# Performance work log

Measured on AMD Instinct MI355X. Metric: run time of the kernel, lower is better.

The kernel has to match this reference:

```python
import jax, jax.numpy as jnp
import numpy as np

DEPTH = 4
DIM = 1024
HEADS = 16
DIM_HEAD = 64
INNER = HEADS * DIM_HEAD  # 1024
MLP = 4096
CTX = 768
SCALE = DIM_HEAD ** -0.5
EPS = 1e-5


def setup_inputs() -> dict:
    key = jax.random.key(0)
    ks = jax.random.split(key, 12)
    def rn(k, shape, s=0.02):
        return jax.random.normal(k, shape, jnp.float32) * s
    return {
        "x": jax.random.normal(ks[0], (2, 2048, DIM), jnp.float32),
        "context": jax.random.normal(ks[1], (2, 1024, CTX), jnp.float32),
        "ln1_g": jnp.ones((DEPTH, DIM), jnp.float32),
        "ln1_b": jnp.zeros((DEPTH, DIM), jnp.float32),
        "w_qkv": rn(ks[2], (DEPTH, DIM, 3 * INNER)),
        "w_sa_o": rn(ks[3], (DEPTH, INNER, DIM)),
        "b_sa_o": jnp.zeros((DEPTH, DIM), jnp.float32),
        "ln2_g": jnp.ones((DEPTH, DIM), jnp.float32),
        "ln2_b": jnp.zeros((DEPTH, DIM), jnp.float32),
        "w_q": rn(ks[4], (DEPTH, DIM, INNER)),
        "w_kv": rn(ks[5], (DEPTH, CTX, 2 * INNER)),
        "w_ca_o": rn(ks[6], (DEPTH, INNER, DIM)),
        "b_ca_o": jnp.zeros((DEPTH, DIM), jnp.float32),
        "ln3_g": jnp.ones((DEPTH, DIM), jnp.float32),
        "ln3_b": jnp.zeros((DEPTH, DIM), jnp.float32),
        "w_ff1": rn(ks[7], (DEPTH, DIM, MLP)),
        "b_ff1": jnp.zeros((DEPTH, MLP), jnp.float32),
        "w_ff2": rn(ks[8], (DEPTH, MLP, DIM)),
        "b_ff2": jnp.zeros((DEPTH, DIM), jnp.float32),
    }


def _ln(x, g, b):
    mu = jnp.mean(x, axis=-1, keepdims=True)
    var = jnp.mean(jnp.square(x - mu), axis=-1, keepdims=True)
    return (x - mu) * jax.lax.rsqrt(var + EPS) * g + b


def _heads(t):
    # [b, n, h*d] -> [b, h, n, d]
    b, n, _ = t.shape
    return t.reshape(b, n, HEADS, DIM_HEAD).transpose(0, 2, 1, 3)


def _mha(q, k, v):
    # q,k,v: [b, h, n, d]; naive matmul-softmax-matmul, same math as the torch code
    attn = jax.nn.softmax(jnp.einsum('bhqd,bhkd->bhqk', q, k) * SCALE, axis=-1)
    out = jnp.einsum('bhqk,bhkd->bhqd', attn, v)
    b, h, n, d = out.shape
    return out.transpose(0, 2, 1, 3).reshape(b, n, h * d)


def reference(x, context, ln1_g, ln1_b, w_qkv, w_sa_o, b_sa_o,
              ln2_g, ln2_b, w_q, w_kv, w_ca_o, b_ca_o,
              ln3_g, ln3_b, w_ff1, b_ff1, w_ff2, b_ff2):
    for i in range(DEPTH):
        # self-attention
        h = _ln(x, ln1_g[i], ln1_b[i])
        qkv = h @ w_qkv[i]
        q, k, v = jnp.split(qkv, 3, axis=-1)
        sa = _mha(_heads(q), _heads(k), _heads(v)) @ w_sa_o[i] + b_sa_o[i]
        x = sa + x
        # cross-attention
        h = _ln(x, ln2_g[i], ln2_b[i])
        q = h @ w_q[i]
        kv = context @ w_kv[i]
        k, v = jnp.split(kv, 2, axis=-1)
        ca = _mha(_heads(q), _heads(k), _heads(v)) @ w_ca_o[i] + b_ca_o[i]
        x = ca + x
        # feed-forward (exact GELU, matching torch nn.GELU default)
        h = _ln(x, ln3_g[i], ln3_b[i])
        ff = jax.nn.gelu(h @ w_ff1[i] + b_ff1[i], approximate=False) @ w_ff2[i] + b_ff2[i]
        x = ff + x
    return x
```

## Files before the change

### kernel.cpp

```cpp
#include <hip/hip_runtime.h>
#include <hip/hip_bf16.h>
#include <math.h>

typedef __bf16 bf16_t;
typedef __bf16 bf16x8 __attribute__((ext_vector_type(8)));
typedef __bf16 bf16x4 __attribute__((ext_vector_type(4)));
typedef float f32x4 __attribute__((ext_vector_type(4)));
typedef unsigned short u16;
typedef unsigned int u32;
typedef u16 u16x8 __attribute__((ext_vector_type(8)));

#define NDEPTH 4
#define DIM 1024
#define NHEADS 16
#define MLP_DIM 4096
#define CTXD 768
#define NTOK 4096
#define NCTX 2048
#define ATT_SCALE 0.125f

__device__ inline void gload_lds16(const void* g, void* l) {
  __builtin_amdgcn_global_load_lds(
      (const __attribute__((address_space(1))) void*)g,
      (__attribute__((address_space(3))) void*)l, 16, 0, 0);
}

__device__ inline u32 packbf2(float a, float b) {
  union { bf16_t h[2]; u32 w; } u;
  u.h[0] = (bf16_t)a; u.h[1] = (bf16_t)b;
  return u.w;
}

template<int EPI>
__device__ inline void epi_store(void* outp, const float* bias, const float* res,
                                 int row, int col, int N, float v) {
  size_t idx = (size_t)row * N + col;
  if (EPI == 3) {
    ((float*)outp)[idx] = v + bias[col] + res[idx];
  } else if (EPI == 2) {
    float vb = v + bias[col];
    ((bf16_t*)outp)[idx] = (bf16_t)(0.5f * vb * (1.f + erff(vb * 0.70710678118f)));
  } else {
    ((bf16_t*)outp)[idx] = (bf16_t)v;
  }
}

template<int EPI>
__global__ __launch_bounds__(512) void gemm_bf16(
    const bf16_t* __restrict__ A, const bf16_t* __restrict__ Bt,
    const float* __restrict__ bias, const float* __restrict__ res,
    void* __restrict__ outp, int M, int N, int K)
{
  __shared__ alignas(16) bf16_t As[3][128 * 32];
  __shared__ alignas(16) bf16_t Bs[3][128 * 32];
  const int tid = threadIdx.x, lane = tid & 63, wave = tid >> 6;
  const int bx = blockIdx.x, by = blockIdx.y;
  const int wr = wave >> 2, wc = wave & 3;
  const int l15 = lane & 15, l4 = lane >> 4;

  const bf16_t* Ag = A + (size_t)by * 128 * K;
  const bf16_t* Bg = Bt + (size_t)bx * 128 * K;

  f32x4 acc[4][2] = {};

  const int srow = tid >> 2, soff = (tid & 3) * 8;
  auto stage = [&](int buf, int k0) {
    gload_lds16(Ag + (size_t)srow * K + k0 + soff, &As[buf][(size_t)tid * 8]);
    gload_lds16(Bg + (size_t)srow * K + k0 + soff, &Bs[buf][(size_t)tid * 8]);
  };

  const int nk = K >> 5;
  stage(0, 0);
  stage(1, 32);
  asm volatile("s_waitcnt vmcnt(2)" ::: "memory");
  __builtin_amdgcn_s_barrier();
  __builtin_amdgcn_sched_barrier(0);

  for (int t = 0; t < nk; ++t) {
    const int cur = t % 3;
    if (t + 2 < nk) stage((t + 2) % 3, (t + 2) << 5);

    bf16x8 af[4], bfr[2];
#pragma unroll
    for (int mi = 0; mi < 4; ++mi)
      af[mi] = *(const bf16x8*)&As[cur][(wr * 64 + mi * 16 + l15) * 32 + l4 * 8];
#pragma unroll
    for (int ni = 0; ni < 2; ++ni)
      bfr[ni] = *(const bf16x8*)&Bs[cur][(wc * 32 + ni * 16 + l15) * 32 + l4 * 8];
#pragma unroll
    for (int mi = 0; mi < 4; ++mi)
#pragma unroll
      for (int ni = 0; ni < 2; ++ni)
        acc[mi][ni] = __builtin_amdgcn_mfma_f32_16x16x32_bf16(af[mi], bfr[ni], acc[mi][ni], 0, 0, 0);

    if (t + 2 < nk) {
      asm volatile("s_waitcnt vmcnt(2)" ::: "memory");
    } else if (t + 1 < nk) {
      asm volatile("s_waitcnt vmcnt(0)" ::: "memory");
    } else {
      break;
    }
    __builtin_amdgcn_s_barrier();
    __builtin_amdgcn_sched_barrier(0);
  }

  const int r0 = by * 128 + wr * 64, c0 = bx * 128 + wc * 32;
#pragma unroll
  for (int ni = 0; ni < 2; ++ni)
#pragma unroll
    for (int mi = 0; mi < 4; ++mi)
#pragma unroll
      for (int r = 0; r < 4; ++r)
        epi_store<EPI>(outp, bias, res, r0 + mi * 16 + l4 * 4 + r,
                       c0 + ni * 16 + l15, N, acc[mi][ni][r]);
}

template<int EPI>
__global__ __launch_bounds__(256) void gemm64_bf16(
    const bf16_t* __restrict__ A, const bf16_t* __restrict__ Bt,
    const float* __restrict__ bias, const float* __restrict__ res,
    void* __restrict__ outp, int M, int N, int K)
{
  __shared__ alignas(16) bf16_t As[3][64 * 32];
  __shared__ alignas(16) bf16_t Bs[3][64 * 32];
  const int tid = threadIdx.x, lane = tid & 63, wave = tid >> 6;
  const int bx = blockIdx.x, by = blockIdx.y;
  const int wr = wave >> 1, wc = wave & 1;
  const int l15 = lane & 15, l4 = lane >> 4;

  const bf16_t* Ag = A + (size_t)by * 64 * K;
  const bf16_t* Bg = Bt + (size_t)bx * 64 * K;

  f32x4 acc[2][2] = {};

  const int srow = tid >> 2, soff = (tid & 3) * 8;
  auto stage = [&](int buf, int k0) {
    gload_lds16(Ag + (size_t)srow * K + k0 + soff, &As[buf][(size_t)tid * 8]);
    gload_lds16(Bg + (size_t)srow * K + k0 + soff, &Bs[buf][(size_t)tid * 8]);
  };

  const int nk = K >> 5;
  stage(0, 0);
  stage(1, 32);
  asm volatile("s_waitcnt vmcnt(2)" ::: "memory");
  __builtin_amdgcn_s_barrier();
  __builtin_amdgcn_sched_barrier(0);

  for (int t = 0; t < nk; ++t) {
    const int cur = t % 3;
    if (t + 2 < nk) stage((t + 2) % 3, (t + 2) << 5);

    bf16x8 af[2], bfr[2];
#pragma unroll
    for (int mi = 0; mi < 2; ++mi)
      af[mi] = *(const bf16x8*)&As[cur][(wr * 32 + mi * 16 + l15) * 32 + l4 * 8];
#pragma unroll
    for (int ni = 0; ni < 2; ++ni)
      bfr[ni] = *(const bf16x8*)&Bs[cur][(wc * 32 + ni * 16 + l15) * 32 + l4 * 8];
#pragma unroll
    for (int mi = 0; mi < 2; ++mi)
#pragma unroll
      for (int ni = 0; ni < 2; ++ni)
        acc[mi][ni] = __builtin_amdgcn_mfma_f32_16x16x32_bf16(af[mi], bfr[ni], acc[mi][ni], 0, 0, 0);

    if (t + 2 < nk) {
      asm volatile("s_waitcnt vmcnt(2)" ::: "memory");
    } else if (t + 1 < nk) {
      asm volatile("s_waitcnt vmcnt(0)" ::: "memory");
    } else {
      break;
    }
    __builtin_amdgcn_s_barrier();
    __builtin_amdgcn_sched_barrier(0);
  }

  const int r0 = by * 64 + wr * 32, c0 = bx * 64 + wc * 32;
#pragma unroll
  for (int ni = 0; ni < 2; ++ni)
#pragma unroll
    for (int mi = 0; mi < 2; ++mi)
#pragma unroll
      for (int r = 0; r < 4; ++r)
        epi_store<EPI>(outp, bias, res, r0 + mi * 16 + l4 * 4 + r,
                       c0 + ni * 16 + l15, N, acc[mi][ni][r]);
}

__global__ __launch_bounds__(512) void attn_fwd(
    const bf16_t* __restrict__ Q, int qs,
    const bf16_t* __restrict__ K, const bf16_t* __restrict__ V, int kvs,
    bf16_t* __restrict__ O, int os, int nq, int nk)
{
  __shared__ bf16_t Ks[2][64][72];
  __shared__ bf16_t Vt[2][64][72];

  const int tid = threadIdx.x, lane = tid & 63, wv = tid >> 6;
  const int l15 = lane & 15, l4 = lane >> 4;
  const int h = blockIdx.y, bz = blockIdx.z;
  const size_t qrow0 = (size_t)bz * nq + (size_t)blockIdx.x * 128;
  const bf16_t* Qb = Q + (qrow0 + wv * 16) * qs + h * 64;
  const bf16_t* Kb = K + (size_t)bz * nk * kvs + h * 64;
  const bf16_t* Vb = V + (size_t)bz * nk * kvs + h * 64;
  bf16_t* Ob = O + (qrow0 + wv * 16) * os + h * 64;

  bf16x8 qa[2];
#pragma unroll
  for (int ks = 0; ks < 2; ++ks)
    qa[ks] = *(const bf16x8*)(Qb + (size_t)l15 * qs + ks * 32 + l4 * 8);

  const int krow = tid >> 3, kcol = (tid & 7) * 8;

  u16x8 kreg, vreg;
  auto load_tile = [&](int kt) {
    kreg = *(const u16x8*)(Kb + (size_t)(kt * 64 + krow) * kvs + kcol);
    u16x8 t;
#pragma unroll
    for (int i = 0; i < 8; ++i)
      t[i] = *(const u16*)(Vb + (size_t)(kt * 64 + wv * 8 + i) * kvs + lane);
    vreg = t;
  };
  auto store_tile = [&](int buf) {
    *(u16x8*)&Ks[buf][krow][kcol] = kreg;
    *(u16x8*)&Vt[buf][lane][wv * 8] = vreg;
  };

  float m_run = -1e30f, l_run = 0.f;
  f32x4 acc[4] = {};

  const int ntiles = nk >> 6;
  load_tile(0);
  store_tile(0);
  __syncthreads();

  for (int kt = 0; kt < ntiles; ++kt) {
    const int cur = kt & 1;
    const bool pre = (kt + 1 < ntiles);
    if (pre) load_tile(kt + 1);

    f32x4 s[4] = {};
#pragma unroll
    for (int ks = 0; ks < 2; ++ks)
#pragma unroll
      for (int f = 0; f < 4; ++f) {
        bf16x8 kf = *(const bf16x8*)&Ks[cur][f * 16 + l15][ks * 32 + l4 * 8];
        s[f] = __builtin_amdgcn_mfma_f32_16x16x32_bf16(kf, qa[ks], s[f], 0, 0, 0);
      }

    float smax = s[0][0];
#pragma unroll
    for (int f = 0; f < 4; ++f)
#pragma unroll
      for (int r = 0; r < 4; ++r) smax = fmaxf(smax, s[f][r]);
    smax = fmaxf(smax, __shfl_xor(smax, 16));
    smax = fmaxf(smax, __shfl_xor(smax, 32));
    smax *= ATT_SCALE;

    if (!__all(smax <= m_run + 8.f)) {
      const float mn = fmaxf(m_run, smax);
      const float esc = __expf(m_run - mn);
      m_run = mn;
      l_run *= esc;
#pragma unroll
      for (int r = 0; r < 4; ++r) {
        float eq = __shfl(esc, (l4 << 4) + (l4 << 2) + r);
#pragma unroll
        for (int d0 = 0; d0 < 4; ++d0) acc[d0][r] *= eq;
      }
    }

    float p[4][4], psum = 0.f;
#pragma unroll
    for (int f = 0; f < 4; ++f)
#pragma unroll
      for (int r = 0; r < 4; ++r) {
        float pv = __expf(s[f][r] * ATT_SCALE - m_run);
        p[f][r] = pv;
        psum += pv;
      }
    psum += __shfl_xor(psum, 16);
    psum += __shfl_xor(psum, 32);
    l_run += psum;

    u32 pk[4][2];
#pragma unroll
    for (int f = 0; f < 4; ++f)
#pragma unroll
      for (int hh = 0; hh < 2; ++hh)
        pk[f][hh] = packbf2(p[f][2 * hh], p[f][2 * hh + 1]);

    bf16x8 pa[2];
#pragma unroll
    for (int ks = 0; ks < 2; ++ks) {
      union { u32 w[4]; bf16x8 v; } pu;
#pragma unroll
      for (int jj = 0; jj < 4; ++jj) {
        int src = l15 + ((((l4 << 1) + (jj >> 1)) & 3) << 4);
        u32 a = (u32)__shfl((int)pk[ks * 2 + 0][jj & 1], src);
        u32 b = (u32)__shfl((int)pk[ks * 2 + 1][jj & 1], src);
        pu.w[jj] = (l4 & 2) ? b : a;
      }
      pa[ks] = pu.v;
    }

#pragma unroll
    for (int ks = 0; ks < 2; ++ks)
#pragma unroll
      for (int d0 = 0; d0 < 4; ++d0) {
        bf16x8 vb = *(const bf16x8*)&Vt[cur][d0 * 16 + l15][ks * 32 + l4 * 8];
        acc[d0] = __builtin_amdgcn_mfma_f32_16x16x32_bf16(pa[ks], vb, acc[d0], 0, 0, 0);
      }

    if (pre) store_tile(cur ^ 1);
    __syncthreads();
  }

#pragma unroll
  for (int r = 0; r < 4; ++r) {
    float lq = __shfl(l_run, (l4 << 4) + (l4 << 2) + r);
    float inv = 1.f / lq;
#pragma unroll
    for (int d0 = 0; d0 < 4; ++d0)
      Ob[(size_t)(l4 * 4 + r) * os + d0 * 16 + l15] = (bf16_t)(acc[d0][r] * inv);
  }
}

__global__ __launch_bounds__(256) void layernorm_f32_bf16(
    const float* __restrict__ x, const float* __restrict__ g, const float* __restrict__ b,
    bf16_t* __restrict__ out)
{
  const int row = blockIdx.x, tid = threadIdx.x;
  const float4 v = ((const float4*)(x + (size_t)row * 1024))[tid];
  float s = v.x + v.y + v.z + v.w;
  float s2 = v.x * v.x + v.y * v.y + v.z * v.z + v.w * v.w;
#pragma unroll
  for (int off = 32; off > 0; off >>= 1) {
    s += __shfl_down(s, off);
    s2 += __shfl_down(s2, off);
  }
  __shared__ float ps[4], ps2[4];
  const int lane = tid & 63, wave = tid >> 6;
  if (lane == 0) { ps[wave] = s; ps2[wave] = s2; }
  __syncthreads();
  s = ps[0] + ps[1] + ps[2] + ps[3];
  s2 = ps2[0] + ps2[1] + ps2[2] + ps2[3];
  const float mu = s * (1.f / 1024.f);
  const float var = s2 * (1.f / 1024.f) - mu * mu;
  const float rstd = rsqrtf(var + 1e-5f);
  const float4 gv = ((const float4*)g)[tid];
  const float4 bv = ((const float4*)b)[tid];
  bf16x4 o;
  o[0] = (bf16_t)((v.x - mu) * rstd * gv.x + bv.x);
  o[1] = (bf16_t)((v.y - mu) * rstd * gv.y + bv.y);
  o[2] = (bf16_t)((v.z - mu) * rstd * gv.z + bv.z);
  o[3] = (bf16_t)((v.w - mu) * rstd * gv.w + bv.w);
  *(bf16x4*)(out + (size_t)row * 1024 + tid * 4) = o;
}

__global__ void transpose_to_bf16(const float* __restrict__ src, bf16_t* __restrict__ dst, int K, int N)
{
  __shared__ float tile[32][33];
  const size_t loff = (size_t)blockIdx.z * K * N;
  src += loff; dst += loff;
  const int k0 = blockIdx.y * 32, n0 = blockIdx.x * 32;
  const int tx = threadIdx.x, ty = threadIdx.y;
#pragma unroll
  for (int i = ty; i < 32; i += 8)
    tile[i][tx] = src[(size_t)(k0 + i) * N + n0 + tx];
  __syncthreads();
#pragma unroll
  for (int i = ty; i < 32; i += 8)
    dst[(size_t)(n0 + i) * K + k0 + tx] = (bf16_t)tile[tx][i];
}

__global__ void f32_to_bf16(const float* __restrict__ src, bf16_t* __restrict__ dst, int n4)
{
  int i = blockIdx.x * blockDim.x + threadIdx.x;
  if (i < n4) {
    float4 v = ((const float4*)src)[i];
    bf16x4 o;
    o[0] = (bf16_t)v.x; o[1] = (bf16_t)v.y; o[2] = (bf16_t)v.z; o[3] = (bf16_t)v.w;
    ((bf16x4*)dst)[i] = o;
  }
}

__global__ void copy_f32(const float* __restrict__ src, float* __restrict__ dst, int n4)
{
  int i = blockIdx.x * blockDim.x + threadIdx.x;
  if (i < n4) ((float4*)dst)[i] = ((const float4*)src)[i];
}

extern "C" void kernel_launch(void* const* d_in, const int* in_sizes, int n_in,
                              void* d_out, int out_size, void* d_ws, size_t ws_size,
                              hipStream_t stream)
{
  const float* x      = (const float*)d_in[0];
  const float* ctx    = (const float*)d_in[1];
  const float* ln1_g  = (const float*)d_in[2];
  const float* ln1_b  = (const float*)d_in[3];
  const float* w_qkv  = (const float*)d_in[4];
  const float* w_sa_o = (const float*)d_in[5];
  const float* b_sa_o = (const float*)d_in[6];
  const float* ln2_g  = (const float*)d_in[7];
  const float* ln2_b  = (const float*)d_in[8];
  const float* w_q    = (const float*)d_in[9];
  const float* w_kv   = (const float*)d_in[10];
  const float* w_ca_o = (const float*)d_in[11];
  const float* b_ca_o = (const float*)d_in[12];
  const float* ln3_g  = (const float*)d_in[13];
  const float* ln3_b  = (const float*)d_in[14];
  const float* w_ff1  = (const float*)d_in[15];
  const float* b_ff1  = (const float*)d_in[16];
  const float* w_ff2  = (const float*)d_in[17];
  const float* b_ff2  = (const float*)d_in[18];

  char* p = (char*)d_ws;
  auto alloc = [&](size_t bytes) { char* r = p; p += (bytes + 255) & ~(size_t)255; return r; };
  bf16_t* wqkv_t = (bf16_t*)alloc((size_t)NDEPTH * 3072 * 1024 * 2);
  bf16_t* wsao_t = (bf16_t*)alloc((size_t)NDEPTH * 1024 * 1024 * 2);
  bf16_t* wq_t   = (bf16_t*)alloc((size_t)NDEPTH * 1024 * 1024 * 2);
  bf16_t* wkv_t  = (bf16_t*)alloc((size_t)NDEPTH * 2048 * 768 * 2);
  bf16_t* wcao_t = (bf16_t*)alloc((size_t)NDEPTH * 1024 * 1024 * 2);
  bf16_t* wff1_t = (bf16_t*)alloc((size_t)NDEPTH * 4096 * 1024 * 2);
  bf16_t* wff2_t = (bf16_t*)alloc((size_t)NDEPTH * 1024 * 4096 * 2);
  bf16_t* ctxb   = (bf16_t*)alloc((size_t)NCTX * CTXD * 2);
  float*  xbuf   = (float*)alloc((size_t)NTOK * DIM * 4);
  bf16_t* lnbuf  = (bf16_t*)alloc((size_t)NTOK * DIM * 2);
  bf16_t* bigbuf = (bf16_t*)alloc((size_t)NTOK * 4096 * 2);
  bf16_t* qbuf   = (bf16_t*)alloc((size_t)NTOK * DIM * 2);
  bf16_t* kvbuf  = (bf16_t*)alloc((size_t)NCTX * 2048 * 2);
  if ((size_t)(p - (char*)d_ws) > ws_size) return;

  dim3 tb(32, 8);
  transpose_to_bf16<<<dim3(3072 / 32, 1024 / 32, NDEPTH), tb, 0, stream>>>(w_qkv, wqkv_t, 1024, 3072);
  transpose_to_bf16<<<dim3(1024 / 32, 1024 / 32, NDEPTH), tb, 0, stream>>>(w_sa_o, wsao_t, 1024, 1024);
  transpose_to_bf16<<<dim3(1024 / 32, 1024 / 32, NDEPTH), tb, 0, stream>>>(w_q, wq_t, 1024, 1024);
  transpose_to_bf16<<<dim3(2048 / 32, 768 / 32, NDEPTH), tb, 0, stream>>>(w_kv, wkv_t, 768, 2048);
  transpose_to_bf16<<<dim3(1024 / 32, 1024 / 32, NDEPTH), tb, 0, stream>>>(w_ca_o, wcao_t, 1024, 1024);
  transpose_to_bf16<<<dim3(4096 / 32, 1024 / 32, NDEPTH), tb, 0, stream>>>(w_ff1, wff1_t, 1024, 4096);
  transpose_to_bf16<<<dim3(1024 / 32, 4096 / 32, NDEPTH), tb, 0, stream>>>(w_ff2, wff2_t, 4096, 1024);
  f32_to_bf16<<<(NCTX * CTXD / 4 + 255) / 256, 256, 0, stream>>>(ctx, ctxb, NCTX * CTXD / 4);
  copy_f32<<<(NTOK * DIM / 4 + 255) / 256, 256, 0, stream>>>(x, xbuf, NTOK * DIM / 4);

  for (int i = 0; i < NDEPTH; ++i) {
    layernorm_f32_bf16<<<NTOK, 256, 0, stream>>>(xbuf, ln1_g + i * DIM, ln1_b + i * DIM, lnbuf);
    gemm_bf16<0><<<dim3(3072 / 128, NTOK / 128), 512, 0, stream>>>(
        lnbuf, wqkv_t + (size_t)i * 3072 * 1024, nullptr, nullptr, bigbuf, NTOK, 3072, 1024);
    attn_fwd<<<dim3(2048 / 128, NHEADS, 2), 512, 0, stream>>>(
        bigbuf, 3072, bigbuf + 1024, bigbuf + 2048, 3072, lnbuf, 1024, 2048, 2048);
    gemm64_bf16<3><<<dim3(1024 / 64, NTOK / 64), 256, 0, stream>>>(
        lnbuf, wsao_t + (size_t)i * 1024 * 1024, b_sa_o + i * DIM, xbuf, xbuf, NTOK, 1024, 1024);
    layernorm_f32_bf16<<<NTOK, 256, 0, stream>>>(xbuf, ln2_g + i * DIM, ln2_b + i * DIM, lnbuf);
    gemm64_bf16<0><<<dim3(1024 / 64, NTOK / 64), 256, 0, stream>>>(
        lnbuf, wq_t + (size_t)i * 1024 * 1024, nullptr, nullptr, qbuf, NTOK, 1024, 1024);
    gemm64_bf16<0><<<dim3(2048 / 64, NCTX / 64), 256, 0, stream>>>(
        ctxb, wkv_t + (size_t)i * 2048 * 768, nullptr, nullptr, kvbuf, NCTX, 2048, 768);
    attn_fwd<<<dim3(2048 / 128, NHEADS, 2), 512, 0, stream>>>(
        qbuf, 1024, kvbuf, kvbuf + 1024, 2048, lnbuf, 1024, 2048, 1024);
    gemm64_bf16<3><<<dim3(1024 / 64, NTOK / 64), 256, 0, stream>>>(
        lnbuf, wcao_t + (size_t)i * 1024 * 1024, b_ca_o + i * DIM, xbuf, xbuf, NTOK, 1024, 1024);
    layernorm_f32_bf16<<<NTOK, 256, 0, stream>>>(xbuf, ln3_g + i * DIM, ln3_b + i * DIM, lnbuf);
    gemm_bf16<2><<<dim3(4096 / 128, NTOK / 128), 512, 0, stream>>>(
        lnbuf, wff1_t + (size_t)i * 4096 * 1024, b_ff1 + i * MLP_DIM, nullptr, bigbuf, NTOK, 4096, 1024);
    gemm64_bf16<3><<<dim3(1024 / 64, NTOK / 64), 256, 0, stream>>>(
        bigbuf, wff2_t + (size_t)i * 1024 * 4096, b_ff2 + i * DIM, xbuf, xbuf, NTOK, 1024, 4096);
  }
  copy_f32<<<(NTOK * DIM / 4 + 255) / 256, 256, 0, stream>>>(xbuf, (float*)d_out, NTOK * DIM / 4);
}
```

Measured before the change: 1.803 ms.

## Rewrite attention with 32x32x16 MFMA, 32 rows per wave, exp2 softmax

```diff
diff --git a/kernel.cpp b/kernel.cpp
--- a/kernel.cpp
+++ b/kernel.cpp
@@ -6,9 +6,11 @@
 typedef __bf16 bf16x8 __attribute__((ext_vector_type(8)));
 typedef __bf16 bf16x4 __attribute__((ext_vector_type(4)));
 typedef float f32x4 __attribute__((ext_vector_type(4)));
+typedef float f32x16 __attribute__((ext_vector_type(16)));
 typedef unsigned short u16;
 typedef unsigned int u32;
 typedef u16 u16x8 __attribute__((ext_vector_type(8)));
+typedef u32 u32x4 __attribute__((ext_vector_type(4)));
 
 #define NDEPTH 4
 #define DIM 1024
@@ -17,7 +19,7 @@
 #define CTXD 768
 #define NTOK 4096
 #define NCTX 2048
-#define ATT_SCALE 0.125f
+#define ATT_SC2 0.18033688011112042f
 
 __device__ inline void gload_lds16(const void* g, void* l) {
   __builtin_amdgcn_global_load_lds(
@@ -185,7 +187,7 @@
                        c0 + ni * 16 + l15, N, acc[mi][ni][r]);
 }
 
-__global__ __launch_bounds__(512) void attn_fwd(
+__global__ __launch_bounds__(256) void attn_fwd(
     const bf16_t* __restrict__ Q, int qs,
     const bf16_t* __restrict__ K, const bf16_t* __restrict__ V, int kvs,
     bf16_t* __restrict__ O, int os, int nq, int nk)
@@ -194,37 +196,47 @@
   __shared__ bf16_t Vt[2][64][72];
 
   const int tid = threadIdx.x, lane = tid & 63, wv = tid >> 6;
-  const int l15 = lane & 15, l4 = lane >> 4;
+  const int l31 = lane & 31, hi = lane >> 5;
   const int h = blockIdx.y, bz = blockIdx.z;
-  const size_t qrow0 = (size_t)bz * nq + (size_t)blockIdx.x * 128;
-  const bf16_t* Qb = Q + (qrow0 + wv * 16) * qs + h * 64;
+  const size_t qrow0 = (size_t)bz * nq + (size_t)blockIdx.x * 128 + wv * 32;
+  const bf16_t* Qb = Q + qrow0 * qs + h * 64;
   const bf16_t* Kb = K + (size_t)bz * nk * kvs + h * 64;
   const bf16_t* Vb = V + (size_t)bz * nk * kvs + h * 64;
-  bf16_t* Ob = O + (qrow0 + wv * 16) * os + h * 64;
-
-  bf16x8 qa[2];
-#pragma unroll
-  for (int ks = 0; ks < 2; ++ks)
-    qa[ks] = *(const bf16x8*)(Qb + (size_t)l15 * qs + ks * 32 + l4 * 8);
-
-  const int krow = tid >> 3, kcol = (tid & 7) * 8;
-
-  u16x8 kreg, vreg;
+  bf16_t* Ob = O + qrow0 * os + h * 64;
+
+  bf16x8 qa[4];
+#pragma unroll
+  for (int c = 0; c < 4; ++c)
+    qa[c] = *(const bf16x8*)(Qb + (size_t)l31 * qs + c * 16 + hi * 8);
+
+  const int krow = tid >> 2, kcol = (tid & 3) * 16;
+  const int vd = tid & 63, vkb = tid >> 6;
+
+  u16x8 kreg[2], vreg[2];
   auto load_tile = [&](int kt) {
-    kreg = *(const u16x8*)(Kb + (size_t)(kt * 64 + krow) * kvs + kcol);
-    u16x8 t;
-#pragma unroll
-    for (int i = 0; i < 8; ++i)
-      t[i] = *(const u16*)(Vb + (size_t)(kt * 64 + wv * 8 + i) * kvs + lane);
-    vreg = t;
+#pragma unroll
+    for (int i = 0; i < 2; ++i)
+      kreg[i] = *(const u16x8*)(Kb + (size_t)(kt * 64 + krow) * kvs + kcol + i * 8);
+#pragma unroll
+    for (int i = 0; i < 2; ++i) {
+      u16x8 t;
+#pragma unroll
+      for (int j = 0; j < 8; ++j)
+        t[j] = *(const u16*)(Vb + (size_t)(kt * 64 + vkb * 16 + i * 8 + j) * kvs + vd);
+      vreg[i] = t;
+    }
   };
   auto store_tile = [&](int buf) {
-    *(u16x8*)&Ks[buf][krow][kcol] = kreg;
-    *(u16x8*)&Vt[buf][lane][wv * 8] = vreg;
+#pragma unroll
+    for (int i = 0; i < 2; ++i)
+      *(u16x8*)&Ks[buf][krow][kcol + i * 8] = kreg[i];
+#pragma unroll
+    for (int i = 0; i < 2; ++i)
+      *(u16x8*)&Vt[buf][vd][vkb * 16 + i * 8] = vreg[i];
   };
 
-  float m_run = -1e30f, l_run = 0.f;
-  f32x4 acc[4] = {};
+  float m_run2 = -1e30f, l_run = 0.f;
+  f32x16 acc[2] = {};
 
   const int ntiles = nk >> 6;
   load_tile(0);
@@ -236,90 +248,91 @@
     const bool pre = (kt + 1 < ntiles);
     if (pre) load_tile(kt + 1);
 
-    f32x4 s[4] = {};
-#pragma unroll
-    for (int ks = 0; ks < 2; ++ks)
-#pragma unroll
-      for (int f = 0; f < 4; ++f) {
-        bf16x8 kf = *(const bf16x8*)&Ks[cur][f * 16 + l15][ks * 32 + l4 * 8];
-        s[f] = __builtin_amdgcn_mfma_f32_16x16x32_bf16(kf, qa[ks], s[f], 0, 0, 0);
+    f32x16 s[2] = {};
+    __builtin_amdgcn_s_setprio(1);
+#pragma unroll
+    for (int kb = 0; kb < 2; ++kb)
+#pragma unroll
+      for (int c = 0; c < 4; ++c) {
+        bf16x8 kf = *(const bf16x8*)&Ks[cur][kb * 32 + l31][c * 16 + hi * 8];
+        s[kb] = __builtin_amdgcn_mfma_f32_32x32x16_bf16(kf, qa[c], s[kb], 0, 0, 0);
       }
+    __builtin_amdgcn_s_setprio(0);
 
     float smax = s[0][0];
 #pragma unroll
-    for (int f = 0; f < 4; ++f)
-#pragma unroll
-      for (int r = 0; r < 4; ++r) smax = fmaxf(smax, s[f][r]);
-    smax = fmaxf(smax, __shfl_xor(smax, 16));
+    for (int kb = 0; kb < 2; ++kb)
+#pragma unroll
+      for (int r = 0; r < 16; ++r) smax = fmaxf(smax, s[kb][r]);
+    smax *= ATT_SC2;
     smax = fmaxf(smax, __shfl_xor(smax, 32));
-    smax *= ATT_SCALE;
-
-    if (!__all(smax <= m_run + 8.f)) {
-      const float mn = fmaxf(m_run, smax);
-      const float esc = __expf(m_run - mn);
-      m_run = mn;
+
+    if (!__all(smax <= m_run2 + 11.0f)) {
+      const float mn = fmaxf(m_run2, smax);
+      const float esc = exp2f(m_run2 - mn);
+      m_run2 = mn;
       l_run *= esc;
 #pragma unroll
-      for (int r = 0; r < 4; ++r) {
-        float eq = __shfl(esc, (l4 << 4) + (l4 << 2) + r);
-#pragma unroll
-        for (int d0 = 0; d0 < 4; ++d0) acc[d0][r] *= eq;
+      for (int r = 0; r < 16; ++r) {
+        int q = (r & 3) + 8 * (r >> 2) + 4 * hi;
+        float eq = __shfl(esc, q);
+        acc[0][r] *= eq;
+        acc[1][r] *= eq;
       }
     }
 
-    float p[4][4], psum = 0.f;
-#pragma unroll
-    for (int f = 0; f < 4; ++f)
-#pragma unroll
-      for (int r = 0; r < 4; ++r) {
-        float pv = __expf(s[f][r] * ATT_SCALE - m_run);
-        p[f][r] = pv;
-        psum += pv;
+    float psum = 0.f;
+    u32x4 paw[2][2];
+#pragma unroll
+    for (int kb = 0; kb < 2; ++kb) {
+      float pv[16];
+#pragma unroll
+      for (int r = 0; r < 16; ++r) {
+        pv[r] = exp2f(s[kb][r] * ATT_SC2 - m_run2);
+        psum += pv[r];
       }
-    psum += __shfl_xor(psum, 16);
+#pragma unroll
+      for (int h2 = 0; h2 < 2; ++h2) {
+        u32 a0 = packbf2(pv[h2 * 8 + 0], pv[h2 * 8 + 1]);
+        u32 a1 = packbf2(pv[h2 * 8 + 2], pv[h2 * 8 + 3]);
+        u32 a2 = packbf2(pv[h2 * 8 + 4], pv[h2 * 8 + 5]);
+        u32 a3 = packbf2(pv[h2 * 8 + 6], pv[h2 * 8 + 7]);
+        asm volatile("v_permlane32_swap_b32 %0, %1" : "+v"(a0), "+v"(a2));
+        asm volatile("v_permlane32_swap_b32 %0, %1" : "+v"(a1), "+v"(a3));
+        paw[kb][h2][0] = a0; paw[kb][h2][1] = a1;
+        paw[kb][h2][2] = a2; paw[kb][h2][3] = a3;
+      }
+    }
     psum += __shfl_xor(psum, 32);
     l_run += psum;
 
-    u32 pk[4][2];
-#pragma unroll
-    for (int f = 0; f < 4; ++f)
-#pragma unroll
-      for (int hh = 0; hh < 2; ++hh)
-        pk[f][hh] = packbf2(p[f][2 * hh], p[f][2 * hh + 1]);
-
-    bf16x8 pa[2];
-#pragma unroll
-    for (int ks = 0; ks < 2; ++ks) {
-      union { u32 w[4]; bf16x8 v; } pu;
-#pragma unroll
-      for (int jj = 0; jj < 4; ++jj) {
-        int src = l15 + ((((l4 << 1) + (jj >> 1)) & 3) << 4);
-        u32 a = (u32)__shfl((int)pk[ks * 2 + 0][jj & 1], src);
-        u32 b = (u32)__shfl((int)pk[ks * 2 + 1][jj & 1], src);
-        pu.w[jj] = (l4 & 2) ? b : a;
+    __builtin_amdgcn_s_setprio(1);
+#pragma unroll
+    for (int kb = 0; kb < 2; ++kb)
+#pragma unroll
+      for (int h2 = 0; h2 < 2; ++h2) {
+        union { u32x4 w; bf16x8 v; } pu;
+        pu.w = paw[kb][h2];
+#pragma unroll
+        for (int dblk = 0; dblk < 2; ++dblk) {
+          bf16x8 vb = *(const bf16x8*)&Vt[cur][dblk * 32 + l31][kb * 32 + h2 * 16 + hi * 8];
+          acc[dblk] = __builtin_amdgcn_mfma_f32_32x32x16_bf16(pu.v, vb, acc[dblk], 0, 0, 0);
+        }
       }
-      pa[ks] = pu.v;
-    }
-
-#pragma unroll
-    for (int ks = 0; ks < 2; ++ks)
-#pragma unroll
-      for (int d0 = 0; d0 < 4; ++d0) {
-        bf16x8 vb = *(const bf16x8*)&Vt[cur][d0 * 16 + l15][ks * 32 + l4 * 8];
-        acc[d0] = __builtin_amdgcn_mfma_f32_16x16x32_bf16(pa[ks], vb, acc[d0], 0, 0, 0);
-      }
+    __builtin_amdgcn_s_setprio(0);
 
     if (pre) store_tile(cur ^ 1);
     __syncthreads();
   }
 
 #pragma unroll
-  for (int r = 0; r < 4; ++r) {
-    float lq = __shfl(l_run, (l4 << 4) + (l4 << 2) + r);
+  for (int r = 0; r < 16; ++r) {
+    int q = (r & 3) + 8 * (r >> 2) + 4 * hi;
+    float lq = __shfl(l_run, q);
     float inv = 1.f / lq;
 #pragma unroll
-    for (int d0 = 0; d0 < 4; ++d0)
-      Ob[(size_t)(l4 * 4 + r) * os + d0 * 16 + l15] = (bf16_t)(acc[d0][r] * inv);
+    for (int dblk = 0; dblk < 2; ++dblk)
+      Ob[(size_t)q * os + dblk * 32 + l31] = (bf16_t)(acc[dblk][r] * inv);
   }
 }
 
@@ -444,7 +457,7 @@
     layernorm_f32_bf16<<<NTOK, 256, 0, stream>>>(xbuf, ln1_g + i * DIM, ln1_b + i * DIM, lnbuf);
     gemm_bf16<0><<<dim3(3072 / 128, NTOK / 128), 512, 0, stream>>>(
         lnbuf, wqkv_t + (size_t)i * 3072 * 1024, nullptr, nullptr, bigbuf, NTOK, 3072, 1024);
-    attn_fwd<<<dim3(2048 / 128, NHEADS, 2), 512, 0, stream>>>(
+    attn_fwd<<<dim3(2048 / 128, NHEADS, 2), 256, 0, stream>>>(
         bigbuf, 3072, bigbuf + 1024, bigbuf + 2048, 3072, lnbuf, 1024, 2048, 2048);
     gemm64_bf16<3><<<dim3(1024 / 64, NTOK / 64), 256, 0, stream>>>(
         lnbuf, wsao_t + (size_t)i * 1024 * 1024, b_sa_o + i * DIM, xbuf, xbuf, NTOK, 1024, 1024);
@@ -453,7 +466,7 @@
         lnbuf, wq_t + (size_t)i * 1024 * 1024, nullptr, nullptr, qbuf, NTOK, 1024, 1024);
     gemm64_bf16<0><<<dim3(2048 / 64, NCTX / 64), 256, 0, stream>>>(
         ctxb, wkv_t + (size_t)i * 2048 * 768, nullptr, nullptr, kvbuf, NCTX, 2048, 768);
-    attn_fwd<<<dim3(2048 / 128, NHEADS, 2), 512, 0, stream>>>(
+    attn_fwd<<<dim3(2048 / 128, NHEADS, 2), 256, 0, stream>>>(
         qbuf, 1024, kvbuf, kvbuf + 1024, 2048, lnbuf, 1024, 2048, 1024);
     gemm64_bf16<3><<<dim3(1024 / 64, NTOK / 64), 256, 0, stream>>>(
         lnbuf, wcao_t + (size_t)i * 1024 * 1024, b_ca_o + i * DIM, xbuf, xbuf, NTOK, 1024, 1024);
```

New measurement: 1.830 ms. About the same (+1.5%).
